# Kernel tuning notes

Hardware: AMD Instinct MI355X
Metric: run time of the kernel (lower is better)

The kernel has to match this reference:

```python
import math
import jax, jax.numpy as jnp
import numpy as np

EMBED_SIZE = 768
HEAD_SIZE = 64


def setup_inputs() -> dict:
    key = jax.random.key(0)
    kx, kq, kk, kv = jax.random.split(key, 4)
    B, S = 4, 4096
    s = 1.0 / math.sqrt(EMBED_SIZE)
    x = jax.random.normal(kx, (B, S, EMBED_SIZE), dtype=jnp.float32)
    # nn.Linear(embed, head, bias=False): y = x @ W.T with W [head, embed]
    Wq = jax.random.uniform(kq, (HEAD_SIZE, EMBED_SIZE), dtype=jnp.float32, minval=-s, maxval=s)
    Wk = jax.random.uniform(kk, (HEAD_SIZE, EMBED_SIZE), dtype=jnp.float32, minval=-s, maxval=s)
    Wv = jax.random.uniform(kv, (HEAD_SIZE, EMBED_SIZE), dtype=jnp.float32, minval=-s, maxval=s)
    return {"x": x, "Wq": Wq, "Wk": Wk, "Wv": Wv}


def reference(x, Wq, Wk, Wv):
    # q,k,v: [B, S, H]
    q = jnp.einsum("bse,he->bsh", x, Wq)
    k = jnp.einsum("bse,he->bsh", x, Wk)
    v = jnp.einsum("bse,he->bsh", x, Wv)
    # NOTE: original uses `//` (floor division) by sqrt(head_size)
    scores = jnp.floor(jnp.einsum("bqh,bkh->bqk", q, k) / math.sqrt(HEAD_SIZE))
    attn = jax.nn.softmax(scores, axis=-1)
    return jnp.einsum("bqk,bkh->bqh", attn, v)
```

## Files before the change

kernel.cpp:

```cpp
#include <hip/hip_runtime.h>
#include <math.h>
#include <stdint.h>

#define B 4
#define S 4096
#define E 768
#define H 64
#define NMAT 192

typedef _Float16 half_t;
typedef __attribute__((ext_vector_type(8))) _Float16 half8;
typedef __attribute__((ext_vector_type(4))) _Float16 half4;
typedef __attribute__((ext_vector_type(4))) float f32x4;
typedef __attribute__((ext_vector_type(16))) float f32x16;

#define LOG2E 1.4426950408889634f

__global__ __launch_bounds__(256) void wprep_kernel(
    const float* __restrict__ Wq, const float* __restrict__ Wk,
    const float* __restrict__ Wv, half_t* __restrict__ Wst)
{
    int gid = blockIdx.x * 256 + threadIdx.x;
    int m = gid / (H * E);
    int rem = gid - m * (H * E);
    int h = rem / E;
    int e = rem - h * E;
    const float* W = (m == 0) ? Wq : (m == 1) ? Wk : Wv;
    float val = W[h * E + e];
    half_t hi = (half_t)val;
    float lo = val - (float)hi;
    int n = m * H + h;
    int ks = e >> 5, kk = e & 31;
    size_t base = ((size_t)(ks * NMAT + n) * 2) * 32 + kk;
    Wst[base]      = hi;
    Wst[base + 32] = (half_t)lo;
}

#define WROW 72
__global__ __launch_bounds__(512, 4) void proj_kernel(
    const float* __restrict__ x, const half_t* __restrict__ Wst,
    half_t* __restrict__ qhi, half_t* __restrict__ qlo,
    half_t* __restrict__ khi, half_t* __restrict__ klo,
    half_t* __restrict__ vt)
{
    __shared__ __align__(16) half_t W_s[2][NMAT * WROW];

    const int t = threadIdx.x;
    const int w = t >> 6, lane = t & 63;
    const int col = lane & 15, quad = lane >> 4;
    const int nsplit = w & 3, msub = w >> 2;
    const int mrow = blockIdx.x * 32 + msub * 16 + col;

    half8 stg[4];
    f32x4 acc[3];
    #pragma unroll
    for (int i = 0; i < 3; ++i) acc[i] = (f32x4){0.f, 0.f, 0.f, 0.f};

    if (t < 384) {
        const half_t* src = Wst + ((size_t)0 * NMAT * 2 + t) * 32;
        #pragma unroll
        for (int i = 0; i < 4; ++i) stg[i] = *(const half8*)(src + i * 8);
        half_t* dst = &W_s[0][(t >> 1) * WROW + (t & 1) * 32];
        #pragma unroll
        for (int i = 0; i < 4; ++i) *(half8*)(dst + i * 8) = stg[i];
    }
    __syncthreads();

    for (int ks = 0; ks < 24; ++ks) {
        const int cur = ks & 1;
        if (ks < 23 && t < 384) {
            const half_t* src = Wst + ((size_t)(ks + 1) * NMAT * 2 + t) * 32;
            #pragma unroll
            for (int i = 0; i < 4; ++i) stg[i] = *(const half8*)(src + i * 8);
        }

        const float* xp = x + (size_t)mrow * E + ks * 32 + quad * 8;
        float4 xa = *(const float4*)xp;
        float4 xb = *(const float4*)(xp + 4);
        float xv[8] = {xa.x, xa.y, xa.z, xa.w, xb.x, xb.y, xb.z, xb.w};
        half8 ah, al;
        #pragma unroll
        for (int j = 0; j < 8; ++j) {
            half_t hi = (half_t)xv[j];
            ah[j] = hi;
            al[j] = (half_t)(xv[j] - (float)hi);
        }

        #pragma unroll
        for (int ci = 0; ci < 3; ++ci) {
            int c = nsplit + ci * 4;
            const half_t* wr = &W_s[cur][(c * 16 + col) * WROW];
            half8 bh = *(const half8*)(wr + quad * 8);
            acc[ci] = __builtin_amdgcn_mfma_f32_16x16x32_f16(ah, bh, acc[ci], 0, 0, 0);
            if (ci < 2) {
                half8 bl = *(const half8*)(wr + 32 + quad * 8);
                acc[ci] = __builtin_amdgcn_mfma_f32_16x16x32_f16(al, bh, acc[ci], 0, 0, 0);
                acc[ci] = __builtin_amdgcn_mfma_f32_16x16x32_f16(ah, bl, acc[ci], 0, 0, 0);
            }
        }

        if (ks < 23 && t < 384) {
            half_t* dst = &W_s[cur ^ 1][(t >> 1) * WROW + (t & 1) * 32];
            #pragma unroll
            for (int i = 0; i < 4; ++i) *(half8*)(dst + i * 8) = stg[i];
        }
        __syncthreads();
    }

    const int srow0 = blockIdx.x * 32 + msub * 16 + quad * 4;
    const int hcol = nsplit * 16 + col;
    #pragma unroll
    for (int r = 0; r < 4; ++r) {
        int srow = srow0 + r;
        float vq = acc[0][r];
        half_t hq = (half_t)vq;
        qhi[(size_t)srow * H + hcol] = hq;
        qlo[(size_t)srow * H + hcol] = (half_t)(vq - (float)hq);
        float vk = acc[1][r];
        half_t hk = (half_t)vk;
        khi[(size_t)srow * H + hcol] = hk;
        klo[(size_t)srow * H + hcol] = (half_t)(vk - (float)hk);
    }
    {
        half4 pk;
        #pragma unroll
        for (int r = 0; r < 4; ++r) pk[r] = (half_t)acc[2][r];
        int bb = srow0 >> 12, s0 = srow0 & (S - 1);
        *(half4*)(vt + ((size_t)(bb * H + hcol)) * S + s0) = pk;
    }
}

__global__ __launch_bounds__(512, 2) void flash_kernel(
    const half_t* __restrict__ qhi, const half_t* __restrict__ qlo,
    const half_t* __restrict__ khi, const half_t* __restrict__ klo,
    const half_t* __restrict__ vt, float* __restrict__ out)
{
    __shared__ __align__(16) char smem[114688];

    const int t = threadIdx.x;
    const int w = t >> 6, lane = t & 63;
    const int n32 = lane & 31, l5 = lane >> 5;
    const int qsub = w & 1, ksw = w >> 1;

    const int b = blockIdx.x >> 6;
    const int qtile = blockIdx.x & 63;
    const int qrow0 = b * S + qtile * 64;
    const int wrow0 = qrow0 + qsub * 32;

    half_t* p_s = (half_t*)(smem + 98304);

    half8 qh[4], ql[4];
    #pragma unroll
    for (int ks = 0; ks < 4; ++ks) {
        size_t off = (size_t)(wrow0 + n32) * H + ks * 16 + l5 * 8;
        qh[ks] = *(const half8*)(qhi + off);
        ql[ks] = *(const half8*)(qlo + off);
    }

    f32x16 O[2];
    #pragma unroll
    for (int i = 0; i < 2; ++i)
        #pragma unroll
        for (int r = 0; r < 16; ++r) O[i][r] = 0.f;
    float lacc[16];
    #pragma unroll
    for (int r = 0; r < 16; ++r) lacc[r] = 0.f;

    const half_t* kh_g = khi + (size_t)b * S * H;
    const half_t* kl_g = klo + (size_t)b * S * H;
    const half_t* vt_g = vt + (size_t)b * H * S;

    half8 stg[6];

    auto load_tile = [&](int kt) {
        #pragma unroll
        for (int i = 0; i < 6; ++i) {
            int f = t + 512 * i;
            const half_t* src;
            if (i < 2) {
                int keyl = f >> 3, p = f & 7, c = p ^ (keyl & 7);
                src = kh_g + (size_t)(kt * 128 + keyl) * H + c * 8;
            } else if (i < 4) {
                int f2 = f - 1024;
                int keyl = f2 >> 3, p = f2 & 7, c = p ^ (keyl & 7);
                src = kl_g + (size_t)(kt * 128 + keyl) * H + c * 8;
            } else {
                int f2 = f - 2048;
                int dim = f2 >> 4, p = f2 & 15, c = p ^ (dim & 15);
                src = vt_g + (size_t)dim * S + kt * 128 + c * 8;
            }
            stg[i] = *(const half8*)src;
        }
    };
    auto store_tile = [&](int buf) {
        half_t* base = (half_t*)(smem + buf * 49152);
        #pragma unroll
        for (int i = 0; i < 6; ++i) {
            int f = t + 512 * i;
            int sec = f >> 10, f2 = f & 1023;
            int off;
            if (sec < 2) off = sec * 8192 + (f2 >> 3) * 64 + (f2 & 7) * 8;
            else         off = 16384 + (f2 >> 4) * 128 + (f2 & 15) * 8;
            *(half8*)(base + off) = stg[i];
        }
    };

    load_tile(0);
    store_tile(0);
    __syncthreads();

    const int keyl = ksw * 32 + n32;
    const int pc = keyl >> 3, po = keyl & 7;
    const int prow = qsub * 32 + n32;

    for (int kt = 0; kt < 32; ++kt) {
        const int cur = kt & 1;
        if (kt < 31) load_tile(kt + 1);

        half_t* khs = (half_t*)(smem + cur * 49152);
        half_t* kls = khs + 8192;
        half_t* vts = kls + 8192;

        f32x16 acc;
        #pragma unroll
        for (int r = 0; r < 16; ++r) acc[r] = 0.f;
        #pragma unroll
        for (int ks = 0; ks < 4; ++ks) {
            int phys = ((ks * 2 + l5) ^ (keyl & 7)) * 8;
            half8 bh = *(const half8*)(khs + keyl * 64 + phys);
            half8 bl = *(const half8*)(kls + keyl * 64 + phys);
            acc = __builtin_amdgcn_mfma_f32_32x32x16_f16(qh[ks], bh, acc, 0, 0, 0);
            acc = __builtin_amdgcn_mfma_f32_32x32x16_f16(ql[ks], bh, acc, 0, 0, 0);
            acc = __builtin_amdgcn_mfma_f32_32x32x16_f16(qh[ks], bl, acc, 0, 0, 0);
        }

        #pragma unroll
        for (int r = 0; r < 16; ++r) {
            float sc = floorf(acc[r] * 0.125f);
            float p = exp2f((sc - 8.0f) * LOG2E);
            lacc[r] += p;
            int rowl = qsub * 32 + (r & 3) + 8 * (r >> 2) + 4 * l5;
            p_s[rowl * 128 + ((pc ^ (rowl & 15)) << 3) + po] = (half_t)p;
        }

        #pragma unroll
        for (int ks2 = 0; ks2 < 2; ++ks2) {
            int c = ksw * 4 + ks2 * 2 + l5;
            half8 pf = *(const half8*)(p_s + prow * 128 + ((c ^ (prow & 15)) << 3));
            #pragma unroll
            for (int nct = 0; nct < 2; ++nct) {
                int dim = nct * 32 + n32;
                half8 vf = *(const half8*)(vts + dim * 128 + ((c ^ (dim & 15)) << 3));
                O[nct] = __builtin_amdgcn_mfma_f32_32x32x16_f16(pf, vf, O[nct], 0, 0, 0);
            }
        }

        if (kt < 31) store_tile(cur ^ 1);
        __syncthreads();
    }

    #pragma unroll
    for (int mask = 1; mask <= 16; mask <<= 1) {
        #pragma unroll
        for (int r = 0; r < 16; ++r) lacc[r] += __shfl_xor(lacc[r], mask);
    }

    float* Oc  = (float*)smem;
    float* l_s = (float*)(smem + 65536);
    #pragma unroll
    for (int nct = 0; nct < 2; ++nct) {
        #pragma unroll
        for (int r = 0; r < 16; ++r) {
            int rowl = qsub * 32 + (r & 3) + 8 * (r >> 2) + 4 * l5;
            Oc[(ksw * 64 + rowl) * 64 + nct * 32 + n32] = O[nct][r];
        }
    }
    if (n32 == 0) {
        #pragma unroll
        for (int r = 0; r < 16; ++r) {
            int rowl = qsub * 32 + (r & 3) + 8 * (r >> 2) + 4 * l5;
            l_s[ksw * 64 + rowl] = lacc[r];
        }
    }
    __syncthreads();

    {
        int row = t >> 3;
        int d0 = (t & 7) * 8;
        float den = 0.f;
        float4 na = make_float4(0.f, 0.f, 0.f, 0.f);
        float4 nb = make_float4(0.f, 0.f, 0.f, 0.f);
        #pragma unroll
        for (int k = 0; k < 4; ++k) {
            den += l_s[k * 64 + row];
            const float* oc = Oc + (size_t)(k * 64 + row) * 64 + d0;
            float4 a = *(const float4*)oc;
            float4 bq = *(const float4*)(oc + 4);
            na.x += a.x;  na.y += a.y;  na.z += a.z;  na.w += a.w;
            nb.x += bq.x; nb.y += bq.y; nb.z += bq.z; nb.w += bq.w;
        }
        float inv = 1.f / den;
        float4 o1 = make_float4(na.x * inv, na.y * inv, na.z * inv, na.w * inv);
        float4 o2 = make_float4(nb.x * inv, nb.y * inv, nb.z * inv, nb.w * inv);
        float* op = out + (size_t)(qrow0 + row) * H + d0;
        *(float4*)op = o1;
        *(float4*)(op + 4) = o2;
    }
}

extern "C" void kernel_launch(void* const* d_in, const int* in_sizes, int n_in,
                              void* d_out, int out_size, void* d_ws, size_t ws_size,
                              hipStream_t stream) {
    const float* x  = (const float*)d_in[0];
    const float* Wq = (const float*)d_in[1];
    const float* Wk = (const float*)d_in[2];
    const float* Wv = (const float*)d_in[3];
    float* outp = (float*)d_out;

    const size_t N = (size_t)B * S * H;
    half_t* qhi = (half_t*)d_ws;
    half_t* qlo = qhi + N;
    half_t* khi = qlo + N;
    half_t* klo = khi + N;
    half_t* vt  = klo + N;
    half_t* Wst = vt + N;

    wprep_kernel<<<(3 * H * E) / 256, 256, 0, stream>>>(Wq, Wk, Wv, Wst);
    proj_kernel<<<(B * S) / 32, 512, 0, stream>>>(x, Wst, qhi, qlo, khi, klo, vt);
    flash_kernel<<<B * (S / 64), 512, 0, stream>>>(qhi, qlo, khi, klo, vt, outp);
}
```

Before: 177.4 us.

## Drop LDS weight staging in projection; async global-to-LDS loads in flash kernel

The projection kernel stops staging weights through double-buffered shared memory. Each wave now computes all 12 output column tiles for its own 16 rows and reads weights straight from global/L2, using 256-thread blocks of 64 rows. The flash kernel replaces register-staged K/V tile copies with global_load_lds direct-to-LDS transfers, and loads K-lo fragments straight from global into registers. That shrinks LDS to 80KB so occupancy can rise to 4 blocks per launch bound. This trades LDS traffic and sync for more global/L2 reads and relies on async LDS load ordering via barriers.

```diff
diff --git a/kernel.cpp b/kernel.cpp
--- a/kernel.cpp
+++ b/kernel.cpp
@@ -36,44 +36,22 @@
     Wst[base + 32] = (half_t)lo;
 }
 
-#define WROW 72
-__global__ __launch_bounds__(512, 4) void proj_kernel(
+__global__ __launch_bounds__(256) void proj_kernel(
     const float* __restrict__ x, const half_t* __restrict__ Wst,
     half_t* __restrict__ qhi, half_t* __restrict__ qlo,
     half_t* __restrict__ khi, half_t* __restrict__ klo,
     half_t* __restrict__ vt)
 {
-    __shared__ __align__(16) half_t W_s[2][NMAT * WROW];
-
     const int t = threadIdx.x;
     const int w = t >> 6, lane = t & 63;
     const int col = lane & 15, quad = lane >> 4;
-    const int nsplit = w & 3, msub = w >> 2;
-    const int mrow = blockIdx.x * 32 + msub * 16 + col;
-
-    half8 stg[4];
-    f32x4 acc[3];
-    #pragma unroll
-    for (int i = 0; i < 3; ++i) acc[i] = (f32x4){0.f, 0.f, 0.f, 0.f};
-
-    if (t < 384) {
-        const half_t* src = Wst + ((size_t)0 * NMAT * 2 + t) * 32;
-        #pragma unroll
-        for (int i = 0; i < 4; ++i) stg[i] = *(const half8*)(src + i * 8);
-        half_t* dst = &W_s[0][(t >> 1) * WROW + (t & 1) * 32];
-        #pragma unroll
-        for (int i = 0; i < 4; ++i) *(half8*)(dst + i * 8) = stg[i];
-    }
-    __syncthreads();
+    const int mrow = blockIdx.x * 64 + w * 16 + col;
+
+    f32x4 acc[12];
+    #pragma unroll
+    for (int i = 0; i < 12; ++i) acc[i] = (f32x4){0.f, 0.f, 0.f, 0.f};
 
     for (int ks = 0; ks < 24; ++ks) {
-        const int cur = ks & 1;
-        if (ks < 23 && t < 384) {
-            const half_t* src = Wst + ((size_t)(ks + 1) * NMAT * 2 + t) * 32;
-            #pragma unroll
-            for (int i = 0; i < 4; ++i) stg[i] = *(const half8*)(src + i * 8);
-        }
-
         const float* xp = x + (size_t)mrow * E + ks * 32 + quad * 8;
         float4 xa = *(const float4*)xp;
         float4 xb = *(const float4*)(xp + 4);
@@ -86,56 +64,50 @@
             al[j] = (half_t)(xv[j] - (float)hi);
         }
 
-        #pragma unroll
-        for (int ci = 0; ci < 3; ++ci) {
-            int c = nsplit + ci * 4;
-            const half_t* wr = &W_s[cur][(c * 16 + col) * WROW];
+        const half_t* wbase = Wst + (size_t)ks * (NMAT * 64);
+        #pragma unroll
+        for (int c = 0; c < 12; ++c) {
+            const half_t* wr = wbase + (size_t)(c * 16 + col) * 64;
             half8 bh = *(const half8*)(wr + quad * 8);
-            acc[ci] = __builtin_amdgcn_mfma_f32_16x16x32_f16(ah, bh, acc[ci], 0, 0, 0);
-            if (ci < 2) {
+            acc[c] = __builtin_amdgcn_mfma_f32_16x16x32_f16(ah, bh, acc[c], 0, 0, 0);
+            if (c < 8) {
                 half8 bl = *(const half8*)(wr + 32 + quad * 8);
-                acc[ci] = __builtin_amdgcn_mfma_f32_16x16x32_f16(al, bh, acc[ci], 0, 0, 0);
-                acc[ci] = __builtin_amdgcn_mfma_f32_16x16x32_f16(ah, bl, acc[ci], 0, 0, 0);
+                acc[c] = __builtin_amdgcn_mfma_f32_16x16x32_f16(al, bh, acc[c], 0, 0, 0);
+                acc[c] = __builtin_amdgcn_mfma_f32_16x16x32_f16(ah, bl, acc[c], 0, 0, 0);
             }
         }
-
-        if (ks < 23 && t < 384) {
-            half_t* dst = &W_s[cur ^ 1][(t >> 1) * WROW + (t & 1) * 32];
-            #pragma unroll
-            for (int i = 0; i < 4; ++i) *(half8*)(dst + i * 8) = stg[i];
-        }
-        __syncthreads();
-    }
-
-    const int srow0 = blockIdx.x * 32 + msub * 16 + quad * 4;
-    const int hcol = nsplit * 16 + col;
-    #pragma unroll
-    for (int r = 0; r < 4; ++r) {
-        int srow = srow0 + r;
-        float vq = acc[0][r];
-        half_t hq = (half_t)vq;
-        qhi[(size_t)srow * H + hcol] = hq;
-        qlo[(size_t)srow * H + hcol] = (half_t)(vq - (float)hq);
-        float vk = acc[1][r];
-        half_t hk = (half_t)vk;
-        khi[(size_t)srow * H + hcol] = hk;
-        klo[(size_t)srow * H + hcol] = (half_t)(vk - (float)hk);
-    }
-    {
+    }
+
+    const int srow0 = blockIdx.x * 64 + w * 16 + quad * 4;
+    #pragma unroll
+    for (int c = 0; c < 4; ++c) {
+        const int hcol = c * 16 + col;
+        #pragma unroll
+        for (int r = 0; r < 4; ++r) {
+            int srow = srow0 + r;
+            float vq = acc[c][r];
+            half_t hq = (half_t)vq;
+            qhi[(size_t)srow * H + hcol] = hq;
+            qlo[(size_t)srow * H + hcol] = (half_t)(vq - (float)hq);
+            float vk = acc[c + 4][r];
+            half_t hk = (half_t)vk;
+            khi[(size_t)srow * H + hcol] = hk;
+            klo[(size_t)srow * H + hcol] = (half_t)(vk - (float)hk);
+        }
         half4 pk;
         #pragma unroll
-        for (int r = 0; r < 4; ++r) pk[r] = (half_t)acc[2][r];
+        for (int r = 0; r < 4; ++r) pk[r] = (half_t)acc[c + 8][r];
         int bb = srow0 >> 12, s0 = srow0 & (S - 1);
         *(half4*)(vt + ((size_t)(bb * H + hcol)) * S + s0) = pk;
     }
 }
 
-__global__ __launch_bounds__(512, 2) void flash_kernel(
+__global__ __launch_bounds__(512, 4) void flash_kernel(
     const half_t* __restrict__ qhi, const half_t* __restrict__ qlo,
     const half_t* __restrict__ khi, const half_t* __restrict__ klo,
     const half_t* __restrict__ vt, float* __restrict__ out)
 {
-    __shared__ __align__(16) char smem[114688];
+    __shared__ __align__(16) char smem[81920];
 
     const int t = threadIdx.x;
     const int w = t >> 6, lane = t & 63;
@@ -147,7 +119,7 @@
     const int qrow0 = b * S + qtile * 64;
     const int wrow0 = qrow0 + qsub * 32;
 
-    half_t* p_s = (half_t*)(smem + 98304);
+    half_t* p_s = (half_t*)(smem + 65536);
 
     half8 qh[4], ql[4];
     #pragma unroll
@@ -170,56 +142,59 @@
     const half_t* kl_g = klo + (size_t)b * S * H;
     const half_t* vt_g = vt + (size_t)b * H * S;
 
-    half8 stg[6];
-
-    auto load_tile = [&](int kt) {
-        #pragma unroll
-        for (int i = 0; i < 6; ++i) {
-            int f = t + 512 * i;
-            const half_t* src;
-            if (i < 2) {
-                int keyl = f >> 3, p = f & 7, c = p ^ (keyl & 7);
-                src = kh_g + (size_t)(kt * 128 + keyl) * H + c * 8;
-            } else if (i < 4) {
-                int f2 = f - 1024;
-                int keyl = f2 >> 3, p = f2 & 7, c = p ^ (keyl & 7);
-                src = kl_g + (size_t)(kt * 128 + keyl) * H + c * 8;
-            } else {
-                int f2 = f - 2048;
-                int dim = f2 >> 4, p = f2 & 15, c = p ^ (dim & 15);
-                src = vt_g + (size_t)dim * S + kt * 128 + c * 8;
-            }
-            stg[i] = *(const half8*)src;
+    const char* stage_src[4];
+    int str_tile;
+    uint32_t lds_off;
+    if (w < 4) {
+        int key = w * 32 + (lane >> 3);
+        int c = (lane & 7) ^ (key & 7);
+        const char* b0 = (const char*)kh_g + (size_t)key * 128 + c * 16;
+        #pragma unroll
+        for (int i = 0; i < 4; ++i) stage_src[i] = b0 + i * (8 * 128);
+        str_tile = 128 * 128;
+        lds_off = (uint32_t)w * 4096;
+    } else {
+        #pragma unroll
+        for (int i = 0; i < 4; ++i) {
+            int dim = (w - 4) * 16 + i * 4 + (lane >> 4);
+            int c = (lane & 15) ^ (dim & 15);
+            stage_src[i] = (const char*)vt_g + (size_t)dim * (S * 2) + c * 16;
+        }
+        str_tile = 128 * 2;
+        lds_off = 16384 + (uint32_t)(w - 4) * 4096;
+    }
+
+    auto stage = [&](int kt, int buf) {
+        char* dstb = smem + buf * 32768 + lds_off;
+        #pragma unroll
+        for (int i = 0; i < 4; ++i) {
+            __builtin_amdgcn_global_load_lds(
+                (const __attribute__((address_space(1))) unsigned int*)(stage_src[i] + (size_t)kt * str_tile),
+                (__attribute__((address_space(3))) unsigned int*)(dstb + i * 1024),
+                16, 0, 0);
         }
     };
-    auto store_tile = [&](int buf) {
-        half_t* base = (half_t*)(smem + buf * 49152);
-        #pragma unroll
-        for (int i = 0; i < 6; ++i) {
-            int f = t + 512 * i;
-            int sec = f >> 10, f2 = f & 1023;
-            int off;
-            if (sec < 2) off = sec * 8192 + (f2 >> 3) * 64 + (f2 & 7) * 8;
-            else         off = 16384 + (f2 >> 4) * 128 + (f2 & 15) * 8;
-            *(half8*)(base + off) = stg[i];
-        }
-    };
-
-    load_tile(0);
-    store_tile(0);
-    __syncthreads();
+
+    stage(0, 0);
 
     const int keyl = ksw * 32 + n32;
     const int pc = keyl >> 3, po = keyl & 7;
     const int prow = qsub * 32 + n32;
+    const half_t* klp = kl_g + (size_t)keyl * 64;
 
     for (int kt = 0; kt < 32; ++kt) {
         const int cur = kt & 1;
-        if (kt < 31) load_tile(kt + 1);
-
-        half_t* khs = (half_t*)(smem + cur * 49152);
-        half_t* kls = khs + 8192;
-        half_t* vts = kls + 8192;
+        __syncthreads();
+        if (kt < 31) stage(kt + 1, cur ^ 1);
+
+        const half_t* khs = (const half_t*)(smem + cur * 32768);
+        const half_t* vts = (const half_t*)(smem + cur * 32768 + 16384);
+        const half_t* klrow = klp + (size_t)kt * (128 * 64);
+
+        half8 bl4[4];
+        #pragma unroll
+        for (int ks = 0; ks < 4; ++ks)
+            bl4[ks] = *(const half8*)(klrow + ks * 16 + l5 * 8);
 
         f32x16 acc;
         #pragma unroll
@@ -228,10 +203,9 @@
         for (int ks = 0; ks < 4; ++ks) {
             int phys = ((ks * 2 + l5) ^ (keyl & 7)) * 8;
             half8 bh = *(const half8*)(khs + keyl * 64 + phys);
-            half8 bl = *(const half8*)(kls + keyl * 64 + phys);
             acc = __builtin_amdgcn_mfma_f32_32x32x16_f16(qh[ks], bh, acc, 0, 0, 0);
             acc = __builtin_amdgcn_mfma_f32_32x32x16_f16(ql[ks], bh, acc, 0, 0, 0);
-            acc = __builtin_amdgcn_mfma_f32_32x32x16_f16(qh[ks], bl, acc, 0, 0, 0);
+            acc = __builtin_amdgcn_mfma_f32_32x32x16_f16(qh[ks], bl4[ks], acc, 0, 0, 0);
         }
 
         #pragma unroll
@@ -254,9 +228,6 @@
                 O[nct] = __builtin_amdgcn_mfma_f32_32x32x16_f16(pf, vf, O[nct], 0, 0, 0);
             }
         }
-
-        if (kt < 31) store_tile(cur ^ 1);
-        __syncthreads();
     }
 
     #pragma unroll
@@ -265,6 +236,7 @@
         for (int r = 0; r < 16; ++r) lacc[r] += __shfl_xor(lacc[r], mask);
     }
 
+    __syncthreads();
     float* Oc  = (float*)smem;
     float* l_s = (float*)(smem + 65536);
     #pragma unroll
@@ -326,6 +298,6 @@
     half_t* Wst = vt + N;
 
     wprep_kernel<<<(3 * H * E) / 256, 256, 0, stream>>>(Wq, Wk, Wv, Wst);
-    proj_kernel<<<(B * S) / 32, 512, 0, stream>>>(x, Wst, qhi, qlo, khi, klo, vt);
+    proj_kernel<<<(B * S) / 64, 256, 0, stream>>>(x, Wst, qhi, qlo, khi, klo, vt);
     flash_kernel<<<B * (S / 64), 512, 0, stream>>>(qhi, qlo, khi, klo, vt, outp);
 }
```

After: 293.1 us. 1.65x slower.
